# Performance work log

Hardware: AMD Instinct MI355X
Metric: run time of the kernel (lower is better)

Reference implementation:

```python
import jax, jax.numpy as jnp
import numpy as np

EPS = float(np.finfo(np.float32).tiny)  # matches torch EPSILON
TAU = 0.1
K = 64  # self.k


def setup_inputs() -> dict:
    key = jax.random.key(0)
    k1, k2 = jax.random.split(key)
    bsz, Nmax, ensemble, train_ensemble = 64, 128, 2, 2
    scores = jax.random.normal(k1, (bsz, Nmax, Nmax, ensemble), dtype=jnp.float32)
    # Gumbel(0,1) noise, pre-sampled for determinism: g = -log(-log(U))
    u = jax.random.uniform(k2, (train_ensemble * bsz * ensemble, Nmax * Nmax),
                           dtype=jnp.float32, minval=1e-7, maxval=1.0 - 1e-7)
    gumbel = -jnp.log(-jnp.log(u))
    return {"scores": scores, "gumbel": gumbel, "train_ensemble": train_ensemble}


def reference(scores, gumbel, train_ensemble):
    # policy == 'global_topk_directed'
    bsz, Nmax, _, ensemble = scores.shape
    local_k = min(K, Nmax * Nmax)
    # (bsz, Nmax, Nmax, E) -> (bsz*E, Nmax^2)
    flat = scores.transpose(0, 3, 1, 2).reshape(bsz * ensemble, Nmax * Nmax)
    flat = jnp.tile(flat, (train_ensemble, 1)) + gumbel

    zeros = jnp.zeros_like(flat)

    def step(carry, _):
        f, khot, onehot = carry
        f = f + jnp.log(jnp.maximum(1.0 - onehot, EPS))
        onehot = jax.nn.softmax(f / TAU, axis=1)
        return (f, khot + onehot, onehot), None

    (flat, khot, _), _ = jax.lax.scan(step, (flat, zeros, zeros), None, length=local_k)

    # hard: straight-through k-hot via top-k scatter
    _, ind = jax.lax.top_k(khot, local_k)  # (R, local_k)
    rows = jnp.arange(khot.shape[0])[:, None]
    khot_hard = jnp.zeros_like(khot).at[rows, ind].set(1.0)
    res = khot_hard - jax.lax.stop_gradient(khot) + khot

    new_mask = res.reshape(train_ensemble, bsz, ensemble, Nmax, Nmax).transpose(0, 1, 3, 4, 2)
    return new_mask
```

## Files before the change

kernel.cpp:

```cpp
#include <hip/hip_runtime.h>
#include <math.h>


#define M_ELEMS 16384
#define HALF_N  8192
#define EPT     16
#define KSEL    64
#define NCL     128
#define NCAND   256
#define CPL     4
#define NBINS   4096
#define THRESH_L (HALF_N - NCL)
#define C10     14.42695019f

template <int CTRL, int RM = 0xF>
__device__ __forceinline__ float dpp_f(float x, float identity) {
    return __int_as_float(__builtin_amdgcn_update_dpp(
        __float_as_int(identity), __float_as_int(x), CTRL, RM, 0xF, false));
}
template <int CTRL, int RM = 0xF>
__device__ __forceinline__ unsigned dpp_u(unsigned x, unsigned identity) {
    return (unsigned)__builtin_amdgcn_update_dpp(
        (int)identity, (int)x, CTRL, RM, 0xF, false);
}
__device__ __forceinline__ float wave_sum_bcast(float x) {
    x += dpp_f<0x111>(x, 0.0f);
    x += dpp_f<0x112>(x, 0.0f);
    x += dpp_f<0x114>(x, 0.0f);
    x += dpp_f<0x118>(x, 0.0f);
    x += dpp_f<0x142>(x, 0.0f);
    x += dpp_f<0x143>(x, 0.0f);
    return __int_as_float(__builtin_amdgcn_readlane(__float_as_int(x), 63));
}
__device__ __forceinline__ float wave_fmax_bcast(float x) {
    x = fmaxf(x, dpp_f<0x111>(x, -INFINITY));
    x = fmaxf(x, dpp_f<0x112>(x, -INFINITY));
    x = fmaxf(x, dpp_f<0x114>(x, -INFINITY));
    x = fmaxf(x, dpp_f<0x118>(x, -INFINITY));
    x = fmaxf(x, dpp_f<0x142>(x, -INFINITY));
    x = fmaxf(x, dpp_f<0x143>(x, -INFINITY));
    return __int_as_float(__builtin_amdgcn_readlane(__float_as_int(x), 63));
}
__device__ __forceinline__ unsigned wave_prefix_incl(unsigned x) {
    x += dpp_u<0x111>(x, 0u);
    x += dpp_u<0x112>(x, 0u);
    x += dpp_u<0x114>(x, 0u);
    x += dpp_u<0x118>(x, 0u);
    x += dpp_u<0x142, 0xA>(x, 0u);
    x += dpp_u<0x143, 0xC>(x, 0u);
    return x;
}

__global__ __launch_bounds__(512, 4) void screen_kernel(
    const float* __restrict__ scores,
    const float* __restrict__ gumbel,
    float* __restrict__ cand_f,
    unsigned* __restrict__ cand_i,
    float* __restrict__ out)
{
    const int tid  = threadIdx.x;
    const int lane = tid & 63;
    const int wid  = tid >> 6;
    const int bid  = blockIdx.x;
    const int p    = bid & 255;
    const int half = bid >> 8;
    const int r    = ((p & 127) << 1) | (p >> 7);
    const int t_ = r >> 7;
    const int be = r & 127;
    const int b  = be >> 1;
    const int e  = be & 1;

    __shared__ unsigned int hist[NBINS];
    __shared__ unsigned int wofs[8];
    __shared__ unsigned int cutbin;
    __shared__ unsigned int candcnt;

    float* orow = out + (size_t)(t_ * 64 + b) * (M_ELEMS * 2) + e;

    float fv[EPT];
    {
        const float* gum = gumbel + (size_t)r * M_ELEMS;
        const float* scb = scores + (size_t)b * (M_ELEMS * 2);
        #pragma unroll
        for (int g = 0; g < 4; ++g) {
            const int mb = (half << 13) + (tid << 2) + (g << 11);
            const float4 gv = *reinterpret_cast<const float4*>(&gum[mb]);
            const float4 sa = *reinterpret_cast<const float4*>(&scb[(size_t)mb * 2]);
            const float4 sb = *reinterpret_cast<const float4*>(&scb[(size_t)mb * 2 + 4]);
            float s0, s1, s2, s3;
            if (e == 0) { s0 = sa.x; s1 = sa.z; s2 = sb.x; s3 = sb.z; }
            else        { s0 = sa.y; s1 = sa.w; s2 = sb.y; s3 = sb.w; }
            fv[g * 4 + 0] = s0 + gv.x;
            fv[g * 4 + 1] = s1 + gv.y;
            fv[g * 4 + 2] = s2 + gv.z;
            fv[g * 4 + 3] = s3 + gv.w;
        }
    }
    #pragma unroll
    for (int k = 0; k < NBINS / 512; ++k) hist[tid + k * 512] = 0u;
    __syncthreads();

    #pragma unroll
    for (int k = 0; k < EPT; ++k) {
        const unsigned u  = __float_as_uint(fv[k]);
        const unsigned tk = u ^ (unsigned)(((int)u >> 31) | 0x80000000);
        atomicAdd(&hist[tk >> 20], 1u);
    }
    __syncthreads();

    if (wid == 0) {
        unsigned part = 0;
        #pragma unroll 8
        for (int j = 0; j < 64; ++j)
            part += hist[(lane << 6) + ((j + lane) & 63)];
        const unsigned P = wave_prefix_incl(part);
        const unsigned long long mk = __ballot(P >= THRESH_L);
        const int L = __builtin_ctzll(mk);
        const unsigned base = (L > 0)
            ? (unsigned)__builtin_amdgcn_readlane((int)P, L - 1) : 0u;
        const unsigned h2 = hist[(L << 6) + lane];
        const unsigned p2 = wave_prefix_incl(h2) + base;
        const unsigned long long mk2 = __ballot(p2 >= THRESH_L);
        const int j2 = __builtin_ctzll(mk2);
        if (lane == 0) {
            cutbin  = (unsigned)((L << 6) + j2 + 1);
            candcnt = HALF_N - (unsigned)__builtin_amdgcn_readlane((int)p2, j2);
        }
    }
    __syncthreads();
    const unsigned cutKey = cutbin << 20;
    const unsigned nc     = candcnt;

    unsigned mycnt = 0, hitm = 0;
    #pragma unroll
    for (int k = 0; k < EPT; ++k) {
        const unsigned u  = __float_as_uint(fv[k]);
        const unsigned tk = u ^ (unsigned)(((int)u >> 31) | 0x80000000);
        const bool c = tk >= cutKey;
        hitm |= (c ? 1u : 0u) << k;
        mycnt += c ? 1u : 0u;
    }
    const unsigned inc = wave_prefix_incl(mycnt);
    if (lane == 63) wofs[wid] = inc;
    __syncthreads();
    unsigned wbase = 0;
    #pragma unroll
    for (int i = 0; i < 8; ++i) wbase += (i < wid) ? wofs[i] : 0u;
    unsigned slot = wbase + inc - mycnt;
    const size_t cbase = (size_t)r * NCAND + (size_t)half * NCL;
    #pragma unroll
    for (int k = 0; k < EPT; ++k) {
        if ((hitm >> k) & 1u) {
            cand_f[cbase + slot] = fv[k];
            cand_i[cbase + slot] =
                (unsigned)((half << 13) + (tid << 2) + (k & 3) + ((k >> 2) << 11));
            ++slot;
        }
    }
    if ((unsigned)tid >= nc && tid < NCL) {
        cand_f[cbase + tid] = -INFINITY;
        cand_i[cbase + tid] = 0x7fffffffu;
    }

    #pragma unroll
    for (int k = 0; k < EPT; ++k) {
        const int m = (half << 13) + tid + (k << 9);
        orow[(size_t)m * 2] = 0.0f;
    }
}

__global__ __launch_bounds__(256, 8) void dyn_kernel(
    const float* __restrict__ cand_f,
    const unsigned* __restrict__ cand_i,
    float* __restrict__ out)
{
    const int tid  = threadIdx.x;
    const int lane = tid & 63;
    const int wid  = tid >> 6;
    const int r    = blockIdx.x;
    const int t_ = r >> 7;
    const int be = r & 127;
    const int b  = be >> 1;
    const int e  = be & 1;

    __shared__ __align__(16) float    khbuf[NCAND];
    __shared__ __align__(16) unsigned idxb[NCAND];

    float* orow = out + (size_t)(t_ * 64 + b) * (M_ELEMS * 2) + e;

    idxb[tid] = cand_i[(size_t)r * NCAND + tid];

    if (wid == 0) {
        float cf[CPL], cex[CPL], ckh[CPL];
        #pragma unroll
        for (int k = 0; k < CPL; ++k)
            cf[k] = cand_f[(size_t)r * NCAND + lane + (k << 6)];
        float cmax = fmaxf(fmaxf(cf[0], cf[1]), fmaxf(cf[2], cf[3]));
        cmax = wave_fmax_bcast(cmax);
        const float nbw = fmaf(-cmax, C10, 100.0f);
        #pragma unroll
        for (int k = 0; k < CPL; ++k) {
            cex[k] = __builtin_amdgcn_exp2f(fmaf(cf[k], C10, nbw));
            ckh[k] = 0.0f;
        }
        for (int it = 0; it < KSEL; ++it) {
            float gsum = wave_sum_bcast((cex[0] + cex[1]) + (cex[2] + cex[3]));
            const int eb = (int)((__float_as_uint(gsum) >> 23) & 0xFF);
            if (eb < 127 + 10) {
                int sh = 354 - eb;
                if (sh > 254) sh = 254;
                const float s = __uint_as_float((unsigned)sh << 23);
                #pragma unroll
                for (int k = 0; k < CPL; ++k) cex[k] *= s;
                gsum = wave_sum_bcast((cex[0] + cex[1]) + (cex[2] + cex[3]));
                if (!(gsum > 0.0f)) gsum = INFINITY;
            }
            const float rsum = __builtin_amdgcn_rcpf(gsum);
            #pragma unroll
            for (int k = 0; k < CPL; ++k) {
                ckh[k] = fmaf(cex[k], rsum, ckh[k]);
                const float t  = fmaf(-cex[k], rsum, 1.0f);
                const float t2 = t * t;
                const float t4 = t2 * t2;
                const float t8 = t4 * t4;
                cex[k] = cex[k] * t8 * t2;
            }
        }
        #pragma unroll
        for (int k = 0; k < CPL; ++k) khbuf[lane + (k << 6)] = ckh[k];
    }
    __syncthreads();

    const float    myv = khbuf[tid];
    const unsigned myi = idxb[tid];
    unsigned rank = 0;
    #pragma unroll 8
    for (int j = 0; j < NCAND; j += 4) {
        const float4 v  = *reinterpret_cast<const float4*>(&khbuf[j]);
        const uint4  ii = *reinterpret_cast<const uint4*>(&idxb[j]);
        rank += (v.x > myv || (v.x == myv && ii.x < myi)) ? 1u : 0u;
        rank += (v.y > myv || (v.y == myv && ii.y < myi)) ? 1u : 0u;
        rank += (v.z > myv || (v.z == myv && ii.z < myi)) ? 1u : 0u;
        rank += (v.w > myv || (v.w == myv && ii.w < myi)) ? 1u : 0u;
    }
    if (rank < KSEL && myi < M_ELEMS)
        orow[(size_t)myi * 2] = 1.0f;
}

extern "C" void kernel_launch(void* const* d_in, const int* in_sizes, int n_in,
                              void* d_out, int out_size, void* d_ws, size_t ws_size,
                              hipStream_t stream) {
    const float* scores = (const float*)d_in[0];
    const float* gumbel = (const float*)d_in[1];
    float* out = (float*)d_out;
    const int rows = in_sizes[1] / M_ELEMS;
    float*    cand_f = (float*)d_ws;
    unsigned* cand_i = (unsigned*)d_ws + (size_t)rows * NCAND;
    screen_kernel<<<rows * 2, 512, 0, stream>>>(scores, gumbel, cand_f, cand_i, out);
    dyn_kernel<<<rows, 256, 0, stream>>>(cand_f, cand_i, out);
}
```

Before: 34.18 us.

## Zero output with coalesced float4 stores and run softmax loop redundantly per wave

The screen kernel now zeroes a contiguous 8192-float slice of the output per block using float4 stores, placed before the barrier, instead of strided scalar stores at the end. This relies on the block-to-output mapping covering the whole output contiguously. The dyn kernel has all four waves run the 64-iteration softmax recurrence redundantly, each keeping a private copy of the results in LDS. This removes the block barrier and the idle waves, so each wave ranks its own candidates without waiting. The cost is four times the ALU work per block, a larger LDS footprint, and a lower occupancy bound of 4.

```diff
diff --git a/kernel.cpp b/kernel.cpp
--- a/kernel.cpp
+++ b/kernel.cpp
@@ -65,17 +65,13 @@
     const int p    = bid & 255;
     const int half = bid >> 8;
     const int r    = ((p & 127) << 1) | (p >> 7);
-    const int t_ = r >> 7;
-    const int be = r & 127;
-    const int b  = be >> 1;
-    const int e  = be & 1;
+    const int b    = (r & 127) >> 1;
+    const int e    = r & 1;
 
     __shared__ unsigned int hist[NBINS];
     __shared__ unsigned int wofs[8];
     __shared__ unsigned int cutbin;
     __shared__ unsigned int candcnt;
-
-    float* orow = out + (size_t)(t_ * 64 + b) * (M_ELEMS * 2) + e;
 
     float fv[EPT];
     {
@@ -106,6 +102,14 @@
         const unsigned tk = u ^ (unsigned)(((int)u >> 31) | 0x80000000);
         atomicAdd(&hist[tk >> 20], 1u);
     }
+
+    {
+        float* zs = out + ((size_t)bid << 13);
+        const float4 z4 = make_float4(0.f, 0.f, 0.f, 0.f);
+        #pragma unroll
+        for (int g = 0; g < 4; ++g)
+            *reinterpret_cast<float4*>(&zs[(size_t)(tid + (g << 9)) << 2]) = z4;
+    }
     __syncthreads();
 
     if (wid == 0) {
@@ -161,15 +165,9 @@
         cand_f[cbase + tid] = -INFINITY;
         cand_i[cbase + tid] = 0x7fffffffu;
     }
-
-    #pragma unroll
-    for (int k = 0; k < EPT; ++k) {
-        const int m = (half << 13) + tid + (k << 9);
-        orow[(size_t)m * 2] = 0.0f;
-    }
-}
-
-__global__ __launch_bounds__(256, 8) void dyn_kernel(
+}
+
+__global__ __launch_bounds__(256, 4) void dyn_kernel(
     const float* __restrict__ cand_f,
     const unsigned* __restrict__ cand_i,
     float* __restrict__ out)
@@ -183,61 +181,64 @@
     const int b  = be >> 1;
     const int e  = be & 1;
 
-    __shared__ __align__(16) float    khbuf[NCAND];
-    __shared__ __align__(16) unsigned idxb[NCAND];
+    __shared__ __align__(16) float    khp[4][NCAND];
+    __shared__ __align__(16) unsigned ixp[4][NCAND];
 
     float* orow = out + (size_t)(t_ * 64 + b) * (M_ELEMS * 2) + e;
 
-    idxb[tid] = cand_i[(size_t)r * NCAND + tid];
-
-    if (wid == 0) {
-        float cf[CPL], cex[CPL], ckh[CPL];
-        #pragma unroll
-        for (int k = 0; k < CPL; ++k)
-            cf[k] = cand_f[(size_t)r * NCAND + lane + (k << 6)];
-        float cmax = fmaxf(fmaxf(cf[0], cf[1]), fmaxf(cf[2], cf[3]));
-        cmax = wave_fmax_bcast(cmax);
-        const float nbw = fmaf(-cmax, C10, 100.0f);
+    float cf[CPL], cex[CPL], ckh[CPL];
+    unsigned ci[CPL];
+    #pragma unroll
+    for (int k = 0; k < CPL; ++k) {
+        cf[k] = cand_f[(size_t)r * NCAND + lane + (k << 6)];
+        ci[k] = cand_i[(size_t)r * NCAND + lane + (k << 6)];
+    }
+
+    float cmax = fmaxf(fmaxf(cf[0], cf[1]), fmaxf(cf[2], cf[3]));
+    cmax = wave_fmax_bcast(cmax);
+    const float nbw = fmaf(-cmax, C10, 100.0f);
+    #pragma unroll
+    for (int k = 0; k < CPL; ++k) {
+        cex[k] = __builtin_amdgcn_exp2f(fmaf(cf[k], C10, nbw));
+        ckh[k] = 0.0f;
+    }
+    for (int it = 0; it < KSEL; ++it) {
+        float gsum = wave_sum_bcast((cex[0] + cex[1]) + (cex[2] + cex[3]));
+        const int eb = (int)((__float_as_uint(gsum) >> 23) & 0xFF);
+        if (eb < 127 + 10) {
+            int sh = 354 - eb;
+            if (sh > 254) sh = 254;
+            const float s = __uint_as_float((unsigned)sh << 23);
+            #pragma unroll
+            for (int k = 0; k < CPL; ++k) cex[k] *= s;
+            gsum = wave_sum_bcast((cex[0] + cex[1]) + (cex[2] + cex[3]));
+            if (!(gsum > 0.0f)) gsum = INFINITY;
+        }
+        const float rsum = __builtin_amdgcn_rcpf(gsum);
         #pragma unroll
         for (int k = 0; k < CPL; ++k) {
-            cex[k] = __builtin_amdgcn_exp2f(fmaf(cf[k], C10, nbw));
-            ckh[k] = 0.0f;
-        }
-        for (int it = 0; it < KSEL; ++it) {
-            float gsum = wave_sum_bcast((cex[0] + cex[1]) + (cex[2] + cex[3]));
-            const int eb = (int)((__float_as_uint(gsum) >> 23) & 0xFF);
-            if (eb < 127 + 10) {
-                int sh = 354 - eb;
-                if (sh > 254) sh = 254;
-                const float s = __uint_as_float((unsigned)sh << 23);
-                #pragma unroll
-                for (int k = 0; k < CPL; ++k) cex[k] *= s;
-                gsum = wave_sum_bcast((cex[0] + cex[1]) + (cex[2] + cex[3]));
-                if (!(gsum > 0.0f)) gsum = INFINITY;
-            }
-            const float rsum = __builtin_amdgcn_rcpf(gsum);
-            #pragma unroll
-            for (int k = 0; k < CPL; ++k) {
-                ckh[k] = fmaf(cex[k], rsum, ckh[k]);
-                const float t  = fmaf(-cex[k], rsum, 1.0f);
-                const float t2 = t * t;
-                const float t4 = t2 * t2;
-                const float t8 = t4 * t4;
-                cex[k] = cex[k] * t8 * t2;
-            }
-        }
-        #pragma unroll
-        for (int k = 0; k < CPL; ++k) khbuf[lane + (k << 6)] = ckh[k];
-    }
-    __syncthreads();
-
-    const float    myv = khbuf[tid];
-    const unsigned myi = idxb[tid];
+            ckh[k] = fmaf(cex[k], rsum, ckh[k]);
+            const float t  = fmaf(-cex[k], rsum, 1.0f);
+            const float t2 = t * t;
+            const float t4 = t2 * t2;
+            const float t8 = t4 * t4;
+            cex[k] = cex[k] * t8 * t2;
+        }
+    }
+
+    #pragma unroll
+    for (int k = 0; k < CPL; ++k) {
+        khp[wid][lane + (k << 6)] = ckh[k];
+        ixp[wid][lane + (k << 6)] = ci[k];
+    }
+
+    const float    myv = ckh[wid];
+    const unsigned myi = ci[wid];
     unsigned rank = 0;
     #pragma unroll 8
     for (int j = 0; j < NCAND; j += 4) {
-        const float4 v  = *reinterpret_cast<const float4*>(&khbuf[j]);
-        const uint4  ii = *reinterpret_cast<const uint4*>(&idxb[j]);
+        const float4 v  = *reinterpret_cast<const float4*>(&khp[wid][j]);
+        const uint4  ii = *reinterpret_cast<const uint4*>(&ixp[wid][j]);
         rank += (v.x > myv || (v.x == myv && ii.x < myi)) ? 1u : 0u;
         rank += (v.y > myv || (v.y == myv && ii.y < myi)) ? 1u : 0u;
         rank += (v.z > myv || (v.z == myv && ii.z < myi)) ? 1u : 0u;
```

Result: slower. 37.11 us (+8.6%).
